# Kernel tuning notes

Hardware: AMD Instinct MI355X
Metric: run time of the kernel (lower is better)

Reference implementation:

```python
import jax, jax.numpy as jnp
import numpy as np

B = 8192          # number of analysis windows
N = 4096          # window_size (power of 2, matches radix-2 Cooley-Tukey)


def setup_inputs() -> dict:
    key = jax.random.key(0)
    x = jax.random.normal(key, (B, N), dtype=jnp.float32)
    return {"x": x}


def reference(x):
    """Power spectrum |F(k)|^2 per window.

    The original module implements an exact radix-2 DIT Cooley-Tukey FFT
    (bit-reversal permutation + log2(N) butterfly stages with twiddle
    factors exp(-2*pi*i*k/N)) and returns re^2 + im^2. That is exactly the
    unnormalized DFT, so the clean/efficient faithful form is jnp.fft.fft
    followed by squared magnitude, batched over the leading axis.
    """
    f = jnp.fft.fft(x.astype(jnp.complex64), axis=-1)  # [B, N] complex
    return (jnp.real(f) ** 2 + jnp.imag(f) ** 2).astype(x.dtype)  # [B, N]
```

## Files before the change

### kernel.cpp

```cpp
#include <hip/hip_runtime.h>
#include <math.h>

#define FFT_N   4096
#define NT      256
#define PHYS(i) ((i) + ((i) >> 4))
#define LDS_SZ  (FFT_N + FFT_N / 16)

typedef float f2 __attribute__((ext_vector_type(2)));

__device__ __forceinline__ f2 cmul(f2 a, f2 b) {
    return (f2){a.x, a.x} * b + (f2){-a.y, a.y} * (f2){b.y, b.x};
}

__device__ __forceinline__ void dft4(f2& a, f2& b, f2& c, f2& d) {
    f2 t0 = a + c;
    f2 t1 = a - c;
    f2 t2 = b + d;
    f2 s  = b - d;
    f2 t3 = (f2){s.y, -s.x};
    a = t0 + t2;
    b = t1 + t3;
    c = t0 - t2;
    d = t1 - t3;
}

__device__ __forceinline__ void dft16(f2 v[16]) {
    #pragma unroll
    for (int r1 = 0; r1 < 4; ++r1)
        dft4(v[r1], v[r1 + 4], v[r1 + 8], v[r1 + 12]);

    const float C1 = 0.92387953251128675613f;
    const float S1 = 0.38268343236508977173f;
    const float R2 = 0.70710678118654752440f;
    v[5]  = cmul(v[5],  (f2){ C1, -S1});
    v[9]  = cmul(v[9],  (f2){ R2, -R2});
    v[13] = cmul(v[13], (f2){ S1, -C1});
    v[6]  = cmul(v[6],  (f2){ R2, -R2});
    v[10] = (f2){v[10].y, -v[10].x};
    v[14] = cmul(v[14], (f2){-R2, -R2});
    v[7]  = cmul(v[7],  (f2){ S1, -C1});
    v[11] = cmul(v[11], (f2){-R2, -R2});
    v[15] = cmul(v[15], (f2){-C1,  S1});
    #pragma unroll
    for (int q1 = 0; q1 < 4; ++q1)
        dft4(v[4 * q1], v[4 * q1 + 1], v[4 * q1 + 2], v[4 * q1 + 3]);
}

template <int M>
__device__ __forceinline__ void store_stage_tw(f2* buf, int tid, f2 v[16]) {
    const int j = tid / M;
    const int k = tid % M;
    const int obase = j * 16 * M + k;
    float sn, cs;
    __sincosf((float)j * (-6.28318530717958647692f * (float)M / (float)FFT_N), &sn, &cs);
    f2 w[16];
    w[1]  = (f2){cs, sn};
    w[2]  = cmul(w[1], w[1]);
    w[3]  = cmul(w[2], w[1]);
    w[4]  = cmul(w[2], w[2]);
    w[5]  = cmul(w[4], w[1]);
    w[6]  = cmul(w[4], w[2]);
    w[7]  = cmul(w[4], w[3]);
    w[8]  = cmul(w[4], w[4]);
    w[9]  = cmul(w[8], w[1]);
    w[10] = cmul(w[8], w[2]);
    w[11] = cmul(w[8], w[3]);
    w[12] = cmul(w[8], w[4]);
    w[13] = cmul(w[8], w[5]);
    w[14] = cmul(w[8], w[6]);
    w[15] = cmul(w[8], w[7]);
    buf[PHYS(obase)] = v[0];
    #pragma unroll
    for (int q = 1; q < 16; ++q) {
        const int reg = ((q & 3) << 2) | (q >> 2);
        buf[PHYS(obase + q * M)] = cmul(v[reg], w[q]);
    }
}

__device__ __forceinline__ void load_stage(const f2* buf, int tid, f2 v[16]) {
    #pragma unroll
    for (int r = 0; r < 16; ++r) v[r] = buf[PHYS(tid + 256 * r)];
}

__global__ __launch_bounds__(NT) void spec_fft_kernel(const float* __restrict__ x,
                                                      float* __restrict__ out) {
    __shared__ f2 buf[LDS_SZ];
    const int t = threadIdx.x;
    const size_t base = (size_t)blockIdx.x * (2 * FFT_N);
    const float* __restrict__ x1 = x + base + t;
    const float* __restrict__ x2 = x + base + FFT_N + t;

    f2 v[16];
    #pragma unroll
    for (int r = 0; r < 16; ++r)
        v[r] = (f2){x1[256 * r], x2[256 * r]};

    dft16(v);
    store_stage_tw<1>(buf, t, v);
    __syncthreads();

    load_stage(buf, t, v);
    __syncthreads();
    dft16(v);
    store_stage_tw<16>(buf, t, v);
    __syncthreads();

    load_stage(buf, t, v);
    __syncthreads();
    dft16(v);
    buf[PHYS(t)] = v[0];
    #pragma unroll
    for (int q = 8; q < 16; ++q) {
        const int reg = ((q & 3) << 2) | (q >> 2);
        buf[PHYS(t + 256 * q)] = v[reg];
    }
    __syncthreads();

    float* __restrict__ o1 = out + base;
    float* __restrict__ o2 = out + base + FFT_N;
    #pragma unroll
    for (int q = 0; q < 8; ++q) {
        const int reg = ((q & 3) << 2) | (q >> 2);
        const int k = t + 256 * q;
        const int m = (FFT_N - k) & (FFT_N - 1);
        f2 zk = v[reg];
        f2 zn = buf[PHYS(m)];
        f2 zc = (f2){zn.x, -zn.y};
        f2 e1 = zk + zc;
        f2 e2 = zk - zc;
        float p1 = 0.25f * (e1.x * e1.x + e1.y * e1.y);
        float p2 = 0.25f * (e2.x * e2.x + e2.y * e2.y);
        o1[k] = p1;
        o2[k] = p2;
        o1[m] = p1;
        o2[m] = p2;
    }
    if (t == 0) {
        f2 z = buf[PHYS(2048)];
        o1[2048] = z.x * z.x;
        o2[2048] = z.y * z.y;
    }
}

extern "C" void kernel_launch(void* const* d_in, const int* in_sizes, int n_in,
                              void* d_out, int out_size, void* d_ws, size_t ws_size,
                              hipStream_t stream) {
    const float* x = (const float*)d_in[0];
    float* out = (float*)d_out;
    const int B = in_sizes[0] / FFT_N;
    spec_fft_kernel<<<B / 2, NT, 0, stream>>>(x, out);
}
```

Measured before the change: 46.70 us.

## Process four window pairs per block with double-buffered register prefetch

Each block now handles four pairs of windows instead of one, issuing the global loads for the next pair into a second register array before computing the current pair's FFT. This overlaps global load latency with LDS butterfly work and amortizes block launch overhead. The __syncthreads barriers are replaced by an inline-asm lgkmcnt wait plus s_barrier so outstanding vector-memory prefetches are not drained at each barrier. The cost is double the input register footprint, which may lower occupancy, and four times fewer blocks in the grid.

Result: slower. 48.48 us (+3.8%).

```diff
diff --git a/kernel.cpp b/kernel.cpp
--- a/kernel.cpp
+++ b/kernel.cpp
@@ -3,8 +3,11 @@
 
 #define FFT_N   4096
 #define NT      256
+#define PAIRS   4
 #define PHYS(i) ((i) + ((i) >> 4))
 #define LDS_SZ  (FFT_N + FFT_N / 16)
+
+#define BAR() asm volatile("s_waitcnt lgkmcnt(0)\n\ts_barrier" ::: "memory")
 
 typedef float f2 __attribute__((ext_vector_type(2)));
 
@@ -82,31 +85,28 @@
     for (int r = 0; r < 16; ++r) v[r] = buf[PHYS(tid + 256 * r)];
 }
 
-__global__ __launch_bounds__(NT) void spec_fft_kernel(const float* __restrict__ x,
-                                                      float* __restrict__ out) {
-    __shared__ f2 buf[LDS_SZ];
-    const int t = threadIdx.x;
-    const size_t base = (size_t)blockIdx.x * (2 * FFT_N);
-    const float* __restrict__ x1 = x + base + t;
-    const float* __restrict__ x2 = x + base + FFT_N + t;
-
-    f2 v[16];
+__device__ __forceinline__ void issue_loads(const float* __restrict__ x,
+                                            size_t pair, int t, f2 u[16]) {
+    const float* __restrict__ p = x + pair * (size_t)(2 * FFT_N) + t;
     #pragma unroll
     for (int r = 0; r < 16; ++r)
-        v[r] = (f2){x1[256 * r], x2[256 * r]};
+        u[r] = (f2){p[256 * r], p[FFT_N + 256 * r]};
+}
 
+__device__ __forceinline__ void do_pair(f2* buf, int t, f2 v[16],
+                                        float* __restrict__ out, size_t pair) {
     dft16(v);
     store_stage_tw<1>(buf, t, v);
-    __syncthreads();
+    BAR();
 
     load_stage(buf, t, v);
-    __syncthreads();
+    BAR();
     dft16(v);
     store_stage_tw<16>(buf, t, v);
-    __syncthreads();
+    BAR();
 
     load_stage(buf, t, v);
-    __syncthreads();
+    BAR();
     dft16(v);
     buf[PHYS(t)] = v[0];
     #pragma unroll
@@ -114,10 +114,10 @@
         const int reg = ((q & 3) << 2) | (q >> 2);
         buf[PHYS(t + 256 * q)] = v[reg];
     }
-    __syncthreads();
+    BAR();
 
-    float* __restrict__ o1 = out + base;
-    float* __restrict__ o2 = out + base + FFT_N;
+    float* __restrict__ o1 = out + pair * (size_t)(2 * FFT_N);
+    float* __restrict__ o2 = o1 + FFT_N;
     #pragma unroll
     for (int q = 0; q < 8; ++q) {
         const int reg = ((q & 3) << 2) | (q >> 2);
@@ -140,6 +140,27 @@
         o1[2048] = z.x * z.x;
         o2[2048] = z.y * z.y;
     }
+    BAR();
+}
+
+__global__ __launch_bounds__(NT) void spec_fft_kernel(const float* __restrict__ x,
+                                                      float* __restrict__ out) {
+    __shared__ f2 buf[LDS_SZ];
+    const int t = threadIdx.x;
+    const size_t p0 = (size_t)blockIdx.x * PAIRS;
+
+    f2 A[16], B[16];
+    issue_loads(x, p0, t, A);
+    #pragma unroll
+    for (int p = 0; p < PAIRS; ++p) {
+        if (p & 1) {
+            if (p + 1 < PAIRS) issue_loads(x, p0 + p + 1, t, A);
+            do_pair(buf, t, B, out, p0 + p);
+        } else {
+            if (p + 1 < PAIRS) issue_loads(x, p0 + p + 1, t, B);
+            do_pair(buf, t, A, out, p0 + p);
+        }
+    }
 }
 
 extern "C" void kernel_launch(void* const* d_in, const int* in_sizes, int n_in,
@@ -147,6 +168,6 @@
                               hipStream_t stream) {
     const float* x = (const float*)d_in[0];
     float* out = (float*)d_out;
-    const int B = in_sizes[0] / FFT_N;
-    spec_fft_kernel<<<B / 2, NT, 0, stream>>>(x, out);
+    const int nblk = (in_sizes[0] / FFT_N) / 2 / PAIRS;
+    spec_fft_kernel<<<nblk, NT, 0, stream>>>(x, out);
 }
```

## Halve LDS footprint by exchanging FFT stages in two half-passes

Applied to the files above, without the earlier changes.

Shrinks the shared-memory buffer from about 4352 to 2176 complex entries, so each transpose between radix-16 stages runs in two halves. One half of the threads writes while all threads read half of their inputs, then the other half writes. Twiddles are now applied in registers before the writes, and stage-1 writes use a contiguous 16*t layout. The smaller LDS footprint is meant to fit more workgroups per CU and raise occupancy. The cost is extra barriers and LDS round-trips per stage, plus more registers from the second 16-element array.

Measured after the change: 47.01 us. About the same (+0.6%).

```diff
diff --git a/kernel.cpp b/kernel.cpp
--- a/kernel.cpp
+++ b/kernel.cpp
@@ -3,8 +3,9 @@
 
 #define FFT_N   4096
 #define NT      256
-#define PHYS(i) ((i) + ((i) >> 4))
-#define LDS_SZ  (FFT_N + FFT_N / 16)
+#define HP(i)   ((i) + ((i) >> 4))
+#define LDS_SZ  2176
+#define REG(q)  ((((q) & 3) << 2) | ((q) >> 2))
 
 typedef float f2 __attribute__((ext_vector_type(2)));
 
@@ -47,39 +48,33 @@
 }
 
 template <int M>
-__device__ __forceinline__ void store_stage_tw(f2* buf, int tid, f2 v[16]) {
-    const int j = tid / M;
-    const int k = tid % M;
-    const int obase = j * 16 * M + k;
+__device__ __forceinline__ void twiddle_inplace(int t, f2 v[16]) {
+    const int j = t / M;
     float sn, cs;
     __sincosf((float)j * (-6.28318530717958647692f * (float)M / (float)FFT_N), &sn, &cs);
-    f2 w[16];
-    w[1]  = (f2){cs, sn};
-    w[2]  = cmul(w[1], w[1]);
-    w[3]  = cmul(w[2], w[1]);
-    w[4]  = cmul(w[2], w[2]);
-    w[5]  = cmul(w[4], w[1]);
-    w[6]  = cmul(w[4], w[2]);
-    w[7]  = cmul(w[4], w[3]);
-    w[8]  = cmul(w[4], w[4]);
-    w[9]  = cmul(w[8], w[1]);
-    w[10] = cmul(w[8], w[2]);
-    w[11] = cmul(w[8], w[3]);
-    w[12] = cmul(w[8], w[4]);
-    w[13] = cmul(w[8], w[5]);
-    w[14] = cmul(w[8], w[6]);
-    w[15] = cmul(w[8], w[7]);
-    buf[PHYS(obase)] = v[0];
-    #pragma unroll
-    for (int q = 1; q < 16; ++q) {
-        const int reg = ((q & 3) << 2) | (q >> 2);
-        buf[PHYS(obase + q * M)] = cmul(v[reg], w[q]);
-    }
-}
-
-__device__ __forceinline__ void load_stage(const f2* buf, int tid, f2 v[16]) {
-    #pragma unroll
-    for (int r = 0; r < 16; ++r) v[r] = buf[PHYS(tid + 256 * r)];
+    const f2 w1 = (f2){cs, sn};
+    const f2 w2 = cmul(w1, w1);
+    const f2 w3 = cmul(w2, w1);
+    const f2 w4 = cmul(w2, w2);
+    const f2 w5 = cmul(w4, w1);
+    const f2 w6 = cmul(w4, w2);
+    const f2 w7 = cmul(w4, w3);
+    const f2 w8 = cmul(w4, w4);
+    v[4]  = cmul(v[4],  w1);
+    v[8]  = cmul(v[8],  w2);
+    v[12] = cmul(v[12], w3);
+    v[1]  = cmul(v[1],  w4);
+    v[5]  = cmul(v[5],  w5);
+    v[9]  = cmul(v[9],  w6);
+    v[13] = cmul(v[13], w7);
+    v[2]  = cmul(v[2],  w8);
+    v[6]  = cmul(v[6],  cmul(w8, w1));
+    v[10] = cmul(v[10], cmul(w8, w2));
+    v[14] = cmul(v[14], cmul(w8, w3));
+    v[3]  = cmul(v[3],  cmul(w8, w4));
+    v[7]  = cmul(v[7],  cmul(w8, w5));
+    v[11] = cmul(v[11], cmul(w8, w6));
+    v[15] = cmul(v[15], cmul(w8, w7));
 }
 
 __global__ __launch_bounds__(NT) void spec_fft_kernel(const float* __restrict__ x,
@@ -90,41 +85,65 @@
     const float* __restrict__ x1 = x + base + t;
     const float* __restrict__ x2 = x + base + FFT_N + t;
 
-    f2 v[16];
+    f2 v[16], u[16];
     #pragma unroll
     for (int r = 0; r < 16; ++r)
         v[r] = (f2){x1[256 * r], x2[256 * r]};
 
     dft16(v);
-    store_stage_tw<1>(buf, t, v);
+    twiddle_inplace<1>(t, v);
+    if (t < 128) {
+        #pragma unroll
+        for (int q = 0; q < 16; ++q) buf[HP(16 * t + q)] = v[REG(q)];
+    }
+    __syncthreads();
+    #pragma unroll
+    for (int r = 0; r < 8; ++r) u[r] = buf[HP(t + 256 * r)];
+    __syncthreads();
+    if (t >= 128) {
+        #pragma unroll
+        for (int q = 0; q < 16; ++q) buf[HP(16 * t + q - 2048)] = v[REG(q)];
+    }
+    __syncthreads();
+    #pragma unroll
+    for (int r = 8; r < 16; ++r) u[r] = buf[HP(t + 256 * (r - 8))];
     __syncthreads();
 
-    load_stage(buf, t, v);
+    dft16(u);
+    twiddle_inplace<16>(t, u);
+    const int ob2 = ((t >> 4) << 8) + (t & 15);
+    if (t < 128) {
+        #pragma unroll
+        for (int q = 0; q < 16; ++q) buf[HP(ob2 + 16 * q)] = u[REG(q)];
+    }
     __syncthreads();
-    dft16(v);
-    store_stage_tw<16>(buf, t, v);
+    #pragma unroll
+    for (int r = 0; r < 8; ++r) v[r] = buf[HP(t + 256 * r)];
+    __syncthreads();
+    if (t >= 128) {
+        #pragma unroll
+        for (int q = 0; q < 16; ++q) buf[HP(ob2 + 16 * q - 2048)] = u[REG(q)];
+    }
+    __syncthreads();
+    #pragma unroll
+    for (int r = 8; r < 16; ++r) v[r] = buf[HP(t + 256 * (r - 8))];
     __syncthreads();
 
-    load_stage(buf, t, v);
-    __syncthreads();
     dft16(v);
-    buf[PHYS(t)] = v[0];
     #pragma unroll
-    for (int q = 8; q < 16; ++q) {
-        const int reg = ((q & 3) << 2) | (q >> 2);
-        buf[PHYS(t + 256 * q)] = v[reg];
-    }
+    for (int q = 8; q < 16; ++q) buf[HP(t + 256 * q - 2048)] = v[REG(q)];
     __syncthreads();
 
     float* __restrict__ o1 = out + base;
-    float* __restrict__ o2 = out + base + FFT_N;
+    float* __restrict__ o2 = o1 + FFT_N;
     #pragma unroll
     for (int q = 0; q < 8; ++q) {
-        const int reg = ((q & 3) << 2) | (q >> 2);
         const int k = t + 256 * q;
         const int m = (FFT_N - k) & (FFT_N - 1);
-        f2 zk = v[reg];
-        f2 zn = buf[PHYS(m)];
+        const int mi = (k == 0) ? 0 : (2048 - t - 256 * q);
+        f2 zk = v[REG(q)];
+        f2 zn = buf[HP(mi)];
+        if (k == 0) zn = zk;
         f2 zc = (f2){zn.x, -zn.y};
         f2 e1 = zk + zc;
         f2 e2 = zk - zc;
@@ -136,7 +155,7 @@
         o2[m] = p2;
     }
     if (t == 0) {
-        f2 z = buf[PHYS(2048)];
+        f2 z = buf[HP(0)];
         o1[2048] = z.x * z.x;
         o2[2048] = z.y * z.y;
     }
```
